# Optimization experiments

Hardware: AMD Instinct MI355X
Metric: run time of the kernel (lower is better)

The kernel has to match this reference:

```python
import jax, jax.numpy as jnp
import numpy as np

B, N, H = 512, 100, 768
I = 2 * H  # intermediate_dim default = hidden_dim * 2
NUM_ANS = 16
MAX_ANS = 15
LN_EPS = 1e-5


def setup_inputs() -> dict:
    key = jax.random.key(0)
    ks = jax.random.split(key, 7)
    s = 0.02
    return {
        "v_emb": jax.random.normal(ks[0], (B, N, H), dtype=jnp.float32),
        "W1": jax.random.normal(ks[1], (H, I), dtype=jnp.float32) * s,
        "b1": jax.random.normal(ks[2], (I,), dtype=jnp.float32) * s,
        "gamma": jnp.ones((I,), dtype=jnp.float32),
        "beta": jnp.zeros((I,), dtype=jnp.float32),
        "W2": jax.random.normal(ks[3], (I, 1), dtype=jnp.float32) * s,
        "b2": jax.random.normal(ks[4], (1,), dtype=jnp.float32) * s,
    }


def reference(v_emb, W1, b1, gamma, beta, W2, b2):
    # Linear -> GELU (exact/erf, torch nn.GELU default) -> LayerNorm -> Linear
    h = jnp.einsum("bnh,hi->bni", v_emb, W1) + b1            # [B,N,I]
    h = jax.nn.gelu(h, approximate=False)
    mu = jnp.mean(h, axis=-1, keepdims=True)
    var = jnp.mean(jnp.square(h - mu), axis=-1, keepdims=True)
    h = (h - mu) * jax.lax.rsqrt(var + LN_EPS) * gamma + beta
    scores = jnp.einsum("bni,io->bno", h, W2) + b2           # [B,N,1]
    scores = jax.nn.sigmoid(scores)                           # sigmoid=True branch
    pred = jnp.sum(scores, axis=1)                            # [B,1]
    # pred_to_logits: vectorized round + clamp + one-hot scatter
    # str(int(round(p))) in {'0'..'15'} -> that id; negative -> 0; overflow -> max_ans
    aid = jnp.clip(jnp.round(pred[:, 0]).astype(jnp.int32), 0, MAX_ANS)
    logits = jax.nn.one_hot(aid, NUM_ANS, dtype=scores.dtype)  # [B,16]
    # original returns dict: scores, final_attention_map (==scores), pred, logits
    return scores, pred, logits
```

## Files before the change

kernel.cpp:

```cpp
#include <hip/hip_runtime.h>
#include <hip/hip_bf16.h>
#include <cstdint>
#include <cstddef>

#define BB   512
#define NN   100
#define HH   768
#define II   1536
#define MM   (BB*NN)

typedef __bf16 bf16;
typedef __bf16 bf16x8 __attribute__((ext_vector_type(8)));
typedef float  f32x4  __attribute__((ext_vector_type(4)));

__device__ __forceinline__ void gld_lds16(const bf16* g, bf16* l) {
    __builtin_amdgcn_global_load_lds(
        (const __attribute__((address_space(1))) void*)g,
        (__attribute__((address_space(3))) void*)l, 16, 0, 0);
}

template <int PAT>
__device__ __forceinline__ float swz_add(float x) {
    return x + __int_as_float(
        __builtin_amdgcn_ds_swizzle(__float_as_int(x), PAT));
}
__device__ __forceinline__ float red16(float x) {
    x = swz_add<0x041F>(x);
    x = swz_add<0x081F>(x);
    x = swz_add<0x101F>(x);
    x = swz_add<0x201F>(x);
    return x;
}

__device__ __forceinline__ float fast_gelu(float x) {
    const float ax = fabsf(x) * 0.70710678118654752f;
    const float t  = __builtin_amdgcn_rcpf(fmaf(0.3275911f, ax, 1.0f));
    float p = fmaf(1.061405429f, t, -1.453152027f);
    p = fmaf(p, t, 1.421413741f);
    p = fmaf(p, t, -0.284496736f);
    p = fmaf(p, t, 0.254829592f);
    p = p * t;
    const float e    = __expf(-ax * ax);
    const float erfa = fmaf(-p, e, 1.0f);
    const float erfx = copysignf(erfa, x);
    return 0.5f * x * (1.0f + erfx);
}

__global__ __launch_bounds__(256) void prep_conv(
    const float* __restrict__ v, const float* __restrict__ W1,
    const float* __restrict__ gamma, const float* __restrict__ beta,
    const float* __restrict__ W2, const float* __restrict__ b2,
    bf16* __restrict__ Av, bf16* __restrict__ Wp,
    float* __restrict__ gw, float* __restrict__ scal)
{
    const int bid = blockIdx.x;
    if (bid < 6400) {
        const int r = threadIdx.x >> 5;
        const int j = threadIdx.x & 31;
        const size_t m = (size_t)bid * 8 + r;
        const float* src = v + m * HH;
        bf16* dst = Av + m * HH;
        const int x = (int)((m >> 1) & 3);
        #pragma unroll
        for (int u = 0; u < 3; ++u) {
            const int p = j * 3 + u;
            const int g = (p & ~3) | ((p & 3) ^ x);
            float4 a = *(const float4*)(src + g * 8);
            float4 b = *(const float4*)(src + g * 8 + 4);
            bf16x8 o = { (bf16)a.x,(bf16)a.y,(bf16)a.z,(bf16)a.w,
                         (bf16)b.x,(bf16)b.y,(bf16)b.z,(bf16)b.w };
            *(bf16x8*)(dst + p * 8) = o;
        }
    } else if (bid < 6976) {
        const int t = (bid - 6400) * 256 + threadIdx.x;
        const int n = t % II;
        const int g = t / II;
        const int p = (g & ~3) | ((g & 3) ^ ((n >> 1) & 3));
        bf16x8 o;
        #pragma unroll
        for (int i = 0; i < 8; ++i)
            o[i] = (bf16)W1[(size_t)(g * 8 + i) * II + n];
        *(bf16x8*)&Wp[(size_t)n * HH + p * 8] = o;
    } else if (bid == 6976) {
        for (int j = threadIdx.x; j < II; j += 256)
            gw[j] = gamma[j] * W2[j];
    } else {
        float s1 = 0.f, s2 = 0.f;
        for (int j = threadIdx.x; j < II; j += 256) {
            float w2 = W2[j];
            s1 += gamma[j] * w2;
            s2 += beta[j]  * w2;
        }
        #pragma unroll
        for (int off = 32; off; off >>= 1) {
            s1 += __shfl_down(s1, off, 64);
            s2 += __shfl_down(s2, off, 64);
        }
        __shared__ float a1[4], a2[4];
        int lane = threadIdx.x & 63, w = threadIdx.x >> 6;
        if (lane == 0) { a1[w] = s1; a2[w] = s2; }
        __syncthreads();
        if (threadIdx.x == 0) {
            scal[0] = a1[0] + a1[1] + a1[2] + a1[3];
            scal[1] = a2[0] + a2[1] + a2[2] + a2[3] + b2[0];
        }
    }
}

__global__ __launch_bounds__(256) void gemm_part(
    const bf16* __restrict__ Av, const bf16* __restrict__ Wp,
    const float* __restrict__ b1, const float* __restrict__ gw,
    float* __restrict__ part)
{
    __shared__ bf16  As[2][128 * 32];
    __shared__ bf16  Bs[2][128 * 32];
    __shared__ float sred[2][128][3];

    const int tid  = threadIdx.x;
    const int lin  = (blockIdx.x & 7) * 600 + (blockIdx.x >> 3);
    const int mb   = lin / 12;
    const int nb   = lin % 12;
    const int lane = tid & 63;
    const int w    = tid >> 6;
    const int wm   = w >> 1;
    const int wn   = w & 1;
    const int m15  = lane & 15;
    const int q    = lane >> 4;
    const int row0 = mb * 128;

    const int srow = tid >> 2;
    const int sc   = tid & 3;
    const bf16* aP = Av + (size_t)(row0     + srow) * HH + sc * 8;
    const bf16* bP = Wp + (size_t)(nb * 128 + srow) * HH + sc * 8;
    bf16* asD = &As[0][0] + tid * 8;
    bf16* bsD = &Bs[0][0] + tid * 8;

    const int xsel = (q ^ ((m15 >> 1) & 3)) * 8;

    f32x4 acc[4][4] = {};

    gld_lds16(aP,           asD);
    gld_lds16(aP + 64 * HH, asD + 2048);
    gld_lds16(bP,           bsD);
    gld_lds16(bP + 64 * HH, bsD + 2048);
    asm volatile("s_waitcnt vmcnt(0)" ::: "memory");
    __syncthreads();

    for (int kt = 0; kt < 23; ++kt) {
        const int cur = kt & 1, nxt = cur ^ 1;
        const int ko  = (kt + 1) * 32;

        gld_lds16(aP + ko,           asD + nxt * 4096);
        gld_lds16(aP + ko + 64 * HH, asD + nxt * 4096 + 2048);
        gld_lds16(bP + ko,           bsD + nxt * 4096);
        gld_lds16(bP + ko + 64 * HH, bsD + nxt * 4096 + 2048);

        bf16x8 af[4];
        #pragma unroll
        for (int mt = 0; mt < 4; ++mt)
            af[mt] = *(const bf16x8*)&As[cur][(wm*64 + mt*16 + m15)*32 + xsel];
        #pragma unroll
        for (int nt = 0; nt < 4; ++nt) {
            bf16x8 bfr = *(const bf16x8*)&Bs[cur][(wn*64 + nt*16 + m15)*32 + xsel];
            #pragma unroll
            for (int mt = 0; mt < 4; ++mt)
                acc[mt][nt] = __builtin_amdgcn_mfma_f32_16x16x32_bf16(
                    af[mt], bfr, acc[mt][nt], 0, 0, 0);
        }

        asm volatile("s_waitcnt vmcnt(0)" ::: "memory");
        __syncthreads();
    }
    {
        bf16x8 af[4];
        #pragma unroll
        for (int mt = 0; mt < 4; ++mt)
            af[mt] = *(const bf16x8*)&As[1][(wm*64 + mt*16 + m15)*32 + xsel];
        #pragma unroll
        for (int nt = 0; nt < 4; ++nt) {
            bf16x8 bfr = *(const bf16x8*)&Bs[1][(wn*64 + nt*16 + m15)*32 + xsel];
            #pragma unroll
            for (int mt = 0; mt < 4; ++mt)
                acc[mt][nt] = __builtin_amdgcn_mfma_f32_16x16x32_bf16(
                    af[mt], bfr, acc[mt][nt], 0, 0, 0);
        }
    }

    float bv[4], gv[4];
    #pragma unroll
    for (int nt = 0; nt < 4; ++nt) {
        const int col = nb*128 + wn*64 + nt*16 + m15;
        bv[nt] = b1[col];
        gv[nt] = gw[col];
    }

    #pragma unroll
    for (int mt = 0; mt < 4; ++mt) {
        #pragma unroll
        for (int r = 0; r < 4; ++r) {
            float x0 = 0.f, x1 = 0.f, x2 = 0.f;
            #pragma unroll
            for (int nt = 0; nt < 4; ++nt) {
                float g = fast_gelu(acc[mt][nt][r] + bv[nt]);
                x0 += g; x1 += g * g; x2 += g * gv[nt];
            }
            x0 = red16(x0); x1 = red16(x1); x2 = red16(x2);
            if (m15 == 0) {
                const int rl = wm*64 + mt*16 + q*4 + r;
                sred[wn][rl][0] = x0;
                sred[wn][rl][1] = x1;
                sred[wn][rl][2] = x2;
            }
        }
    }
    __syncthreads();

    if (tid < 128) {
        const size_t rg = (size_t)row0 + tid;
        #pragma unroll
        for (int s = 0; s < 3; ++s)
            part[(size_t)s * 12 * MM + (size_t)nb * MM + rg]
                = sred[0][tid][s] + sred[1][tid][s];
    }
}

__global__ __launch_bounds__(128) void score_pred(
    const float* __restrict__ part, const float* __restrict__ scal,
    float* __restrict__ o_scores, float* __restrict__ o_pred,
    float* __restrict__ o_logits)
{
    const int b = blockIdx.x, t = threadIdx.x;
    float s = 0.f;
    if (t < NN) {
        const size_t row = (size_t)b * NN + t;
        float Sh = 0.f, Shh = 0.f, Shg = 0.f;
        #pragma unroll
        for (int j = 0; j < 12; ++j) {
            Sh  += part[(size_t)0*12*MM + (size_t)j*MM + row];
            Shh += part[(size_t)1*12*MM + (size_t)j*MM + row];
            Shg += part[(size_t)2*12*MM + (size_t)j*MM + row];
        }
        const float mu   = Sh * (1.0f / II);
        const float var  = Shh * (1.0f / II) - mu * mu;
        const float rstd = rsqrtf(var + 1e-5f);
        const float z    = rstd * (Shg - mu * scal[0]) + scal[1];
        s = 1.0f / (1.0f + __expf(-z));
        o_scores[row] = s;
    }
    float v = s;
    #pragma unroll
    for (int off = 32; off; off >>= 1) v += __shfl_down(v, off, 64);
    __shared__ float ssum[2];
    const int lane = t & 63, w = t >> 6;
    if (lane == 0) ssum[w] = v;
    __syncthreads();
    const float p = ssum[0] + ssum[1];
    if (t == 0) o_pred[b] = p;
    if (t < 16) {
        int aid = (int)rintf(p);
        aid = aid < 0 ? 0 : (aid > 15 ? 15 : aid);
        o_logits[b * 16 + t] = (t == aid) ? 1.0f : 0.0f;
    }
}

extern "C" void kernel_launch(void* const* d_in, const int* in_sizes, int n_in,
                              void* d_out, int out_size, void* d_ws, size_t ws_size,
                              hipStream_t stream)
{
    const float* v_emb = (const float*)d_in[0];
    const float* W1    = (const float*)d_in[1];
    const float* b1    = (const float*)d_in[2];
    const float* gamma = (const float*)d_in[3];
    const float* beta  = (const float*)d_in[4];
    const float* W2    = (const float*)d_in[5];
    const float* b2    = (const float*)d_in[6];

    char* ws = (char*)d_ws;
    size_t off = 0;
    bf16*  Wp   = (bf16*)(ws + off);  off += (size_t)II * HH * 2;
    float* gw   = (float*)(ws + off); off += (size_t)II * 4;
    float* scal = (float*)(ws + off); off += 256;
    float* part = (float*)(ws + off); off += (size_t)MM * 36 * 4;
    bf16*  Av   = (bf16*)(ws + off);  off += (size_t)MM * HH * 2;

    float* out       = (float*)d_out;
    float* o_scores  = out;
    float* o_pred    = out + MM;
    float* o_logits  = out + MM + BB;

    hipLaunchKernelGGL(prep_conv, dim3(6978), dim3(256), 0, stream,
                       v_emb, W1, gamma, beta, W2, b2, Av, Wp, gw, scal);
    hipLaunchKernelGGL(gemm_part, dim3((MM / 128) * 12), dim3(256),
                       0, stream, Av, Wp, b1, gw, part);
    hipLaunchKernelGGL(score_pred, dim3(BB), dim3(128), 0, stream,
                       part, scal, o_scores, o_pred, o_logits);
}
```

Measured before the change: 422.7 us.

## Triple-buffer GEMM LDS loads with partial vmcnt waits and MFMA priority

Replaces the double-buffered K loop with a three-stage LDS ring so two tile loads stay in flight while a third is computed. The barrier waits only for the older stage (vmcnt(4)) instead of draining all loads. MFMA blocks are wrapped in s_setprio, and the bf16 conversion kernel now gives each lane consecutive 16-byte chunks per iteration so writes coalesce. This costs more LDS per block, which may lower occupancy, and the barrier no longer waits on LDS reads before the next overwrite.

```diff
diff --git a/kernel.cpp b/kernel.cpp
--- a/kernel.cpp
+++ b/kernel.cpp
@@ -63,7 +63,7 @@
         const int x = (int)((m >> 1) & 3);
         #pragma unroll
         for (int u = 0; u < 3; ++u) {
-            const int p = j * 3 + u;
+            const int p = u * 32 + j;
             const int g = (p & ~3) | ((p & 3) ^ x);
             float4 a = *(const float4*)(src + g * 8);
             float4 b = *(const float4*)(src + g * 8 + 4);
@@ -112,8 +112,8 @@
     const float* __restrict__ b1, const float* __restrict__ gw,
     float* __restrict__ part)
 {
-    __shared__ bf16  As[2][128 * 32];
-    __shared__ bf16  Bs[2][128 * 32];
+    __shared__ bf16  As[3 * 4096];
+    __shared__ bf16  Bs[3 * 4096];
     __shared__ float sred[2][128][3];
 
     const int tid  = threadIdx.x;
@@ -132,59 +132,60 @@
     const int sc   = tid & 3;
     const bf16* aP = Av + (size_t)(row0     + srow) * HH + sc * 8;
     const bf16* bP = Wp + (size_t)(nb * 128 + srow) * HH + sc * 8;
-    bf16* asD = &As[0][0] + tid * 8;
-    bf16* bsD = &Bs[0][0] + tid * 8;
+    bf16* asD = As + tid * 8;
+    bf16* bsD = Bs + tid * 8;
 
     const int xsel = (q ^ ((m15 >> 1) & 3)) * 8;
 
     f32x4 acc[4][4] = {};
 
-    gld_lds16(aP,           asD);
-    gld_lds16(aP + 64 * HH, asD + 2048);
-    gld_lds16(bP,           bsD);
-    gld_lds16(bP + 64 * HH, bsD + 2048);
-    asm volatile("s_waitcnt vmcnt(0)" ::: "memory");
-    __syncthreads();
-
-    for (int kt = 0; kt < 23; ++kt) {
-        const int cur = kt & 1, nxt = cur ^ 1;
-        const int ko  = (kt + 1) * 32;
-
-        gld_lds16(aP + ko,           asD + nxt * 4096);
-        gld_lds16(aP + ko + 64 * HH, asD + nxt * 4096 + 2048);
-        gld_lds16(bP + ko,           bsD + nxt * 4096);
-        gld_lds16(bP + ko + 64 * HH, bsD + nxt * 4096 + 2048);
-
-        bf16x8 af[4];
-        #pragma unroll
-        for (int mt = 0; mt < 4; ++mt)
-            af[mt] = *(const bf16x8*)&As[cur][(wm*64 + mt*16 + m15)*32 + xsel];
-        #pragma unroll
-        for (int nt = 0; nt < 4; ++nt) {
-            bf16x8 bfr = *(const bf16x8*)&Bs[cur][(wn*64 + nt*16 + m15)*32 + xsel];
-            #pragma unroll
-            for (int mt = 0; mt < 4; ++mt)
-                acc[mt][nt] = __builtin_amdgcn_mfma_f32_16x16x32_bf16(
-                    af[mt], bfr, acc[mt][nt], 0, 0, 0);
-        }
-
-        asm volatile("s_waitcnt vmcnt(0)" ::: "memory");
-        __syncthreads();
-    }
-    {
-        bf16x8 af[4];
-        #pragma unroll
-        for (int mt = 0; mt < 4; ++mt)
-            af[mt] = *(const bf16x8*)&As[1][(wm*64 + mt*16 + m15)*32 + xsel];
-        #pragma unroll
-        for (int nt = 0; nt < 4; ++nt) {
-            bf16x8 bfr = *(const bf16x8*)&Bs[1][(wn*64 + nt*16 + m15)*32 + xsel];
-            #pragma unroll
-            for (int mt = 0; mt < 4; ++mt)
-                acc[mt][nt] = __builtin_amdgcn_mfma_f32_16x16x32_bf16(
-                    af[mt], bfr, acc[mt][nt], 0, 0, 0);
-        }
-    }
+#define STAGE(T, BUF) do {                                                  \
+    const bf16* _a = aP + (T) * 32;                                         \
+    const bf16* _b = bP + (T) * 32;                                         \
+    gld_lds16(_a,           asD + (BUF) * 4096);                            \
+    gld_lds16(_a + 64 * HH, asD + (BUF) * 4096 + 2048);                     \
+    gld_lds16(_b,           bsD + (BUF) * 4096);                            \
+    gld_lds16(_b + 64 * HH, bsD + (BUF) * 4096 + 2048);                     \
+} while (0)
+
+#define COMPUTE(BUF) do {                                                   \
+    bf16x8 af[4];                                                           \
+    _Pragma("unroll")                                                       \
+    for (int mt = 0; mt < 4; ++mt)                                          \
+        af[mt] = *(const bf16x8*)&As[(BUF)*4096 + (wm*64 + mt*16 + m15)*32 + xsel]; \
+    __builtin_amdgcn_s_setprio(1);                                          \
+    _Pragma("unroll")                                                       \
+    for (int nt = 0; nt < 4; ++nt) {                                        \
+        bf16x8 bfr = *(const bf16x8*)&Bs[(BUF)*4096 + (wn*64 + nt*16 + m15)*32 + xsel]; \
+        _Pragma("unroll")                                                   \
+        for (int mt = 0; mt < 4; ++mt)                                      \
+            acc[mt][nt] = __builtin_amdgcn_mfma_f32_16x16x32_bf16(          \
+                af[mt], bfr, acc[mt][nt], 0, 0, 0);                         \
+    }                                                                       \
+    __builtin_amdgcn_s_setprio(0);                                          \
+} while (0)
+
+#define WAITBAR(N) do {                                                     \
+    asm volatile("s_waitcnt vmcnt(" #N ")" ::: "memory");                   \
+    __builtin_amdgcn_s_barrier();                                           \
+} while (0)
+
+    STAGE(0, 0);
+    STAGE(1, 1);
+    WAITBAR(4);
+
+    for (int kt = 0; kt < 21; kt += 3) {
+        STAGE(kt + 2, 2); COMPUTE(0); WAITBAR(4);
+        STAGE(kt + 3, 0); COMPUTE(1); WAITBAR(4);
+        STAGE(kt + 4, 1); COMPUTE(2); WAITBAR(4);
+    }
+    STAGE(23, 2); COMPUTE(0); WAITBAR(4);
+    COMPUTE(1); WAITBAR(0);
+    COMPUTE(2);
+
+#undef STAGE
+#undef COMPUTE
+#undef WAITBAR
 
     float bv[4], gv[4];
     #pragma unroll
```

New measurement: 455.7 us. 1.08x slower.

## Widen GEMM K-tile to 64 with single buffer and 8-way XOR swizzle

Applied to the files above, without the earlier changes.

The GEMM main loop now stages a 64-wide K slice per iteration in a single LDS buffer instead of double-buffered 32-wide slices. That halves the number of barrier and wait rounds per tile. The preprocessing kernels change their pre-swizzle of the activation and weight layouts to an 8-chunk XOR pattern to match the wider rows and avoid LDS bank conflicts. The trade-off is that global-to-LDS loads no longer overlap with MFMA compute, since each iteration waits for its loads before computing.

```diff
diff --git a/kernel.cpp b/kernel.cpp
--- a/kernel.cpp
+++ b/kernel.cpp
@@ -60,11 +60,11 @@
         const size_t m = (size_t)bid * 8 + r;
         const float* src = v + m * HH;
         bf16* dst = Av + m * HH;
-        const int x = (int)((m >> 1) & 3);
+        const int x = (int)(m & 7);
         #pragma unroll
         for (int u = 0; u < 3; ++u) {
-            const int p = j * 3 + u;
-            const int g = (p & ~3) | ((p & 3) ^ x);
+            const int p = u * 32 + j;
+            const int g = (p & ~7) | ((p & 7) ^ x);
             float4 a = *(const float4*)(src + g * 8);
             float4 b = *(const float4*)(src + g * 8 + 4);
             bf16x8 o = { (bf16)a.x,(bf16)a.y,(bf16)a.z,(bf16)a.w,
@@ -75,7 +75,7 @@
         const int t = (bid - 6400) * 256 + threadIdx.x;
         const int n = t % II;
         const int g = t / II;
-        const int p = (g & ~3) | ((g & 3) ^ ((n >> 1) & 3));
+        const int p = (g & ~7) | ((g & 7) ^ (n & 7));
         bf16x8 o;
         #pragma unroll
         for (int i = 0; i < 8; ++i)
@@ -112,8 +112,8 @@
     const float* __restrict__ b1, const float* __restrict__ gw,
     float* __restrict__ part)
 {
-    __shared__ bf16  As[2][128 * 32];
-    __shared__ bf16  Bs[2][128 * 32];
+    __shared__ bf16  As[128 * 64];
+    __shared__ bf16  Bs[128 * 64];
     __shared__ float sred[2][128][3];
 
     const int tid  = threadIdx.x;
@@ -128,62 +128,43 @@
     const int q    = lane >> 4;
     const int row0 = mb * 128;
 
-    const int srow = tid >> 2;
-    const int sc   = tid & 3;
+    const int srow = tid >> 3;
+    const int sc   = tid & 7;
     const bf16* aP = Av + (size_t)(row0     + srow) * HH + sc * 8;
     const bf16* bP = Wp + (size_t)(nb * 128 + srow) * HH + sc * 8;
-    bf16* asD = &As[0][0] + tid * 8;
-    bf16* bsD = &Bs[0][0] + tid * 8;
-
-    const int xsel = (q ^ ((m15 >> 1) & 3)) * 8;
+    bf16* asD = As + tid * 8;
+    bf16* bsD = Bs + tid * 8;
 
     f32x4 acc[4][4] = {};
 
-    gld_lds16(aP,           asD);
-    gld_lds16(aP + 64 * HH, asD + 2048);
-    gld_lds16(bP,           bsD);
-    gld_lds16(bP + 64 * HH, bsD + 2048);
-    asm volatile("s_waitcnt vmcnt(0)" ::: "memory");
-    __syncthreads();
-
-    for (int kt = 0; kt < 23; ++kt) {
-        const int cur = kt & 1, nxt = cur ^ 1;
-        const int ko  = (kt + 1) * 32;
-
-        gld_lds16(aP + ko,           asD + nxt * 4096);
-        gld_lds16(aP + ko + 64 * HH, asD + nxt * 4096 + 2048);
-        gld_lds16(bP + ko,           bsD + nxt * 4096);
-        gld_lds16(bP + ko + 64 * HH, bsD + nxt * 4096 + 2048);
-
-        bf16x8 af[4];
-        #pragma unroll
-        for (int mt = 0; mt < 4; ++mt)
-            af[mt] = *(const bf16x8*)&As[cur][(wm*64 + mt*16 + m15)*32 + xsel];
-        #pragma unroll
-        for (int nt = 0; nt < 4; ++nt) {
-            bf16x8 bfr = *(const bf16x8*)&Bs[cur][(wn*64 + nt*16 + m15)*32 + xsel];
+    for (int kt = 0; kt < 12; ++kt) {
+        const int ko = kt * 64;
+        #pragma unroll
+        for (int i = 0; i < 4; ++i)
+            gld_lds16(aP + (size_t)(32 * i) * HH + ko, asD + i * 2048);
+        #pragma unroll
+        for (int i = 0; i < 4; ++i)
+            gld_lds16(bP + (size_t)(32 * i) * HH + ko, bsD + i * 2048);
+        asm volatile("s_waitcnt vmcnt(0)" ::: "memory");
+        __syncthreads();
+
+        #pragma unroll
+        for (int kb = 0; kb < 2; ++kb) {
+            const int xsel = ((kb * 4 + q) ^ (m15 & 7)) * 8;
+            bf16x8 af[4];
             #pragma unroll
             for (int mt = 0; mt < 4; ++mt)
-                acc[mt][nt] = __builtin_amdgcn_mfma_f32_16x16x32_bf16(
-                    af[mt], bfr, acc[mt][nt], 0, 0, 0);
-        }
-
-        asm volatile("s_waitcnt vmcnt(0)" ::: "memory");
+                af[mt] = *(const bf16x8*)&As[(wm*64 + mt*16 + m15)*64 + xsel];
+            #pragma unroll
+            for (int nt = 0; nt < 4; ++nt) {
+                bf16x8 bfr = *(const bf16x8*)&Bs[(wn*64 + nt*16 + m15)*64 + xsel];
+                #pragma unroll
+                for (int mt = 0; mt < 4; ++mt)
+                    acc[mt][nt] = __builtin_amdgcn_mfma_f32_16x16x32_bf16(
+                        af[mt], bfr, acc[mt][nt], 0, 0, 0);
+            }
+        }
         __syncthreads();
-    }
-    {
-        bf16x8 af[4];
-        #pragma unroll
-        for (int mt = 0; mt < 4; ++mt)
-            af[mt] = *(const bf16x8*)&As[1][(wm*64 + mt*16 + m15)*32 + xsel];
-        #pragma unroll
-        for (int nt = 0; nt < 4; ++nt) {
-            bf16x8 bfr = *(const bf16x8*)&Bs[1][(wn*64 + nt*16 + m15)*32 + xsel];
-            #pragma unroll
-            for (int mt = 0; mt < 4; ++mt)
-                acc[mt][nt] = __builtin_amdgcn_mfma_f32_16x16x32_bf16(
-                    af[mt], bfr, acc[mt][nt], 0, 0, 0);
-        }
     }
 
     float bv[4], gv[4];
```

New measurement: 414.8 us. About the same (-1.8%).
